# Kernel tuning notes

Measured on AMD Instinct MI355X. Metric: run time of the kernel, lower is better.

## Reference

```python
import jax, jax.numpy as jnp
import numpy as np
from jax import lax

NUM_ANCHORS = 9
NUM_CLASSES = 80
SPATIALS = [6400, 1600, 400, 100, 25]
FEATS = [80, 40, 20, 10, 5]
STRIDES = [8, 16, 32, 64, 128]
SIZES = [32, 64, 128, 256, 512]
CONF_THR = 0.6
IOU_THR = 0.5
MAX_OUT = 200
MAX_EDGE = 640.0  # max(input_size)
BATCH = 8


def _make_anchors():
    """RetinaNet-style anchors, [sum(s)*9, 4] in x1y1x2y2; anchors for one
    spatial location are contiguous, matching the reshape order in forward."""
    ratios = [0.5, 1.0, 2.0]
    scales = [1.0, 2.0 ** (1.0 / 3.0), 2.0 ** (2.0 / 3.0)]
    out = []
    for st, base, f in zip(STRIDES, SIZES, FEATS):
        wh = np.array([[base * s * np.sqrt(r), base * s / np.sqrt(r)]
                       for r in ratios for s in scales], dtype=np.float64)  # [9,2]
        c = (np.arange(f, dtype=np.float64) + 0.5) * st
        cxg, cyg = np.meshgrid(c, c)
        ctr = np.stack([cxg.ravel(), cyg.ravel()], -1)  # [f*f, 2]
        a = np.concatenate([ctr[:, None, :] - wh[None] / 2,
                            ctr[:, None, :] + wh[None] / 2], -1)  # [f*f, 9, 4]
        out.append(a.reshape(-1, 4))
    return np.concatenate(out, 0).astype(np.float32)


def setup_inputs() -> dict:
    key = jax.random.key(0)
    ks = jax.random.split(key, 10)
    inp = {}
    for i, s in enumerate(SPATIALS):
        inp[f"logits_{i}"] = jax.random.normal(ks[i], (BATCH, NUM_ANCHORS * NUM_CLASSES, s), jnp.float32)
        inp[f"regress_{i}"] = jax.random.normal(ks[5 + i], (BATCH, NUM_ANCHORS * 4, s), jnp.float32) * 0.1
    inp["anchors"] = jnp.asarray(_make_anchors())
    return inp


def _head_reshape(x, s, c):
    # [B, A*c, s] -> [B, s, A*c] -> [B, s*A, c]
    b = x.shape[0]
    return jnp.transpose(x, (0, 2, 1)).reshape(b, s * NUM_ANCHORS, c)


def _decode(anchors, deltas):
    # anchors [A,4] x1y1x2y2, deltas [B,A,4] (dx,dy,dw,dh)
    aw = anchors[:, 2] - anchors[:, 0]
    ah = anchors[:, 3] - anchors[:, 1]
    ax = anchors[:, 0] + 0.5 * aw
    ay = anchors[:, 1] + 0.5 * ah
    cx = ax + deltas[..., 0] * aw
    cy = ay + deltas[..., 1] * ah
    w = aw * jnp.exp(deltas[..., 2])
    h = ah * jnp.exp(deltas[..., 3])
    return jnp.stack([cx - 0.5 * w, cy - 0.5 * h, cx + 0.5 * w, cy + 0.5 * h], -1)


def _nms_single(scores, cats, boxes):
    # scores [A], cats [A] int, boxes [A,4]. Class-aware NMS via class offset
    # (same trick as batch_cls_nms_2d using max_edge): different classes never overlap.
    shifted = boxes + (cats.astype(boxes.dtype) * (2.0 * MAX_EDGE))[:, None]
    areas = (shifted[:, 2] - shifted[:, 0]) * (shifted[:, 3] - shifted[:, 1])
    s0 = jnp.where(scores >= CONF_THR, scores, -1.0)

    def step(s, _):
        idx = jnp.argmax(s)
        sc = s[idx]
        valid = sc > 0.0
        b = shifted[idx]
        ix1 = jnp.maximum(b[0], shifted[:, 0])
        iy1 = jnp.maximum(b[1], shifted[:, 1])
        ix2 = jnp.minimum(b[2], shifted[:, 2])
        iy2 = jnp.minimum(b[3], shifted[:, 3])
        inter = jnp.clip(ix2 - ix1, 0.0) * jnp.clip(iy2 - iy1, 0.0)
        area_b = (b[2] - b[0]) * (b[3] - b[1])
        iou = inter / (area_b + areas - inter + 1e-9)
        suppress = valid & (iou > IOU_THR)
        s = jnp.where(suppress, -1.0, s).at[idx].set(-1.0)
        return s, (idx, jnp.where(valid, sc, 0.0), valid)

    _, (idxs, scs, vs) = lax.scan(step, s0, None, length=MAX_OUT)
    vf = vs.astype(boxes.dtype)
    det_boxes = boxes[idxs] * vf[:, None]
    det_cats = jnp.where(vs, cats[idxs].astype(boxes.dtype), -1.0)
    # dets: [MAX_OUT, 6] = (x1,y1,x2,y2,score,cat); padded rows are zeros / cat=-1
    return jnp.concatenate([det_boxes, scs[:, None], det_cats[:, None]], -1)


def reference(logits_0, logits_1, logits_2, logits_3, logits_4,
              regress_0, regress_1, regress_2, regress_3, regress_4, anchors):
    logits = [logits_0, logits_1, logits_2, logits_3, logits_4]
    regress = [regress_0, regress_1, regress_2, regress_3, regress_4]
    logits = jnp.concatenate([_head_reshape(x, s, NUM_CLASSES)
                              for x, s in zip(logits, SPATIALS)], axis=1)   # [B, A, C]
    regress = jnp.concatenate([_head_reshape(x, s, 4)
                               for x, s in zip(regress, SPATIALS)], axis=1)  # [B, A, 4]
    scores = jax.nn.sigmoid(logits)                   # [B, A, C]
    sc = jnp.max(scores, axis=-1)                     # per-anchor best score
    cats = jnp.argmax(scores, axis=-1)                # per-anchor best class
    boxes = _decode(anchors, regress)                 # [B, A, 4]
    dets = jax.vmap(_nms_single)(sc, cats, boxes)     # [B, MAX_OUT, 6]
    return dets
```

## Files before the change

### kernel.cpp

```cpp
#include <hip/hip_runtime.h>
#include <cmath>

#define A_TOT 76725
#define A_PAD 76728
#define NBATCH 8
#define NCLS 80
#define NANCH 9
#define NOUT 200

#define MCAP 1024
#define NTH 1024
#define NBUCK 4096
#define CHUNK 64
#define NSLC 32
#define KBASE 0x3EC00000u
#define KSHIFT 16
#define NCHUNKS 36

__device__ __forceinline__ void decode_box(int b, int j,
                                           const float* __restrict__ rg0,
                                           const float* __restrict__ rg1,
                                           const float* __restrict__ rg2,
                                           const float* __restrict__ rg3,
                                           const float* __restrict__ rg4,
                                           const float* __restrict__ anchors,
                                           double* __restrict__ o4)
{
    int s, base;
    const float* rg;
    if (j >= 76500)      { s = 25;   base = 76500; rg = rg4; }
    else if (j >= 75600) { s = 100;  base = 75600; rg = rg3; }
    else if (j >= 72000) { s = 400;  base = 72000; rg = rg2; }
    else if (j >= 57600) { s = 1600; base = 57600; rg = rg1; }
    else                 { s = 6400; base = 0;     rg = rg0; }
    const int rem = j - base;
    const int loc = rem / 9;
    const int aa  = rem - loc * 9;
    const size_t ro = ((size_t)(b * NANCH + aa) * 4) * s + loc;
    const float f0 = rg[ro];
    const float f1 = rg[ro + (size_t)s];
    const float f2 = rg[ro + 2 * (size_t)s];
    const float f3 = rg[ro + 3 * (size_t)s];

    double d0 = (double)f0, d1 = (double)f1, d2 = (double)f2, d3 = (double)f3;
    const float4 av = *(const float4*)(anchors + (size_t)j * 4);
    double ax1 = (double)av.x, ay1 = (double)av.y;
    double ax2 = (double)av.z, ay2 = (double)av.w;
    double aw = ax2 - ax1, ah = ay2 - ay1;
    double acx = ax1 + 0.5 * aw, acy = ay1 + 0.5 * ah;
    double cx = acx + d0 * aw, cy = acy + d1 * ah;
    double w = aw * exp(d2), h = ah * exp(d3);
    o4[0] = cx - 0.5 * w;
    o4[1] = cy - 0.5 * h;
    o4[2] = cx + 0.5 * w;
    o4[3] = cy + 0.5 * h;
}

#define CMP4(vv, cc)                                            \
    do {                                                        \
        if ((vv).x > m.x) { m.x = (vv).x; mcx = (cc); }         \
        if ((vv).y > m.y) { m.y = (vv).y; mcy = (cc); }         \
        if ((vv).z > m.z) { m.z = (vv).z; mcz = (cc); }         \
        if ((vv).w > m.w) { m.w = (vv).w; mcw = (cc); }         \
    } while (0)

__global__ __launch_bounds__(512, 4)
void prep_kernel(const float* __restrict__ lg0, const float* __restrict__ lg1,
                 const float* __restrict__ lg2, const float* __restrict__ lg3,
                 const float* __restrict__ lg4,
                 unsigned* __restrict__ keys,
                 unsigned char* __restrict__ cats,
                 unsigned* __restrict__ hist)
{
    const int cx = blockIdx.x;
    const int a  = blockIdx.y;
    const int b  = blockIdx.z;
    int lvl, local;
    if (cx < 25)      { lvl = 0; local = cx; }
    else if (cx < 32) { lvl = 1; local = cx - 25; }
    else if (cx < 34) { lvl = 2; local = cx - 32; }
    else if (cx < 35) { lvl = 3; local = 0; }
    else              { lvl = 4; local = 0; }

    const int   sarr[5] = {6400, 1600, 400, 100, 25};
    const int   barr[5] = {0, 57600, 72000, 75600, 76500};
    const float* lgs[5] = {lg0, lg1, lg2, lg3, lg4};
    const int s = sarr[lvl], base = barr[lvl];
    const float* lg = lgs[lvl];

    __shared__ unsigned lh[NBUCK];
    __shared__ float4   smv[7][64];
    __shared__ int      smc[7][64][4];

    const int tid = threadIdx.x;
    for (int i = tid; i < NBUCK; i += 512) lh[i] = 0u;

    const int t2 = tid & 63;
    const int q  = tid >> 6;
    const int c0 = q * 10;
    const int locbase = local * 256 + t2 * 4;
    const bool act = locbase < s;

    float mj[4]  = {-1e30f, -1e30f, -1e30f, -1e30f};
    int   mcj[4] = {0, 0, 0, 0};

    if (act) {
        const float* lga = lg + ((size_t)(b * NANCH + a) * NCLS) * s + locbase;
        if ((s & 3) == 0) {
            const float* p  = lga + (size_t)c0 * s;
            const size_t ss = (size_t)s;
            float4 v0 = *(const float4*)(p);
            float4 v1 = *(const float4*)(p + ss);
            float4 v2 = *(const float4*)(p + 2 * ss);
            float4 v3 = *(const float4*)(p + 3 * ss);
            float4 v4 = *(const float4*)(p + 4 * ss);
            float4 v5 = *(const float4*)(p + 5 * ss);
            float4 v6 = *(const float4*)(p + 6 * ss);
            float4 v7 = *(const float4*)(p + 7 * ss);
            float4 v8 = *(const float4*)(p + 8 * ss);
            float4 v9 = *(const float4*)(p + 9 * ss);
            float4 m = v0;
            int mcx = c0, mcy = c0, mcz = c0, mcw = c0;
            CMP4(v1, c0 + 1); CMP4(v2, c0 + 2); CMP4(v3, c0 + 3);
            CMP4(v4, c0 + 4); CMP4(v5, c0 + 5); CMP4(v6, c0 + 6);
            CMP4(v7, c0 + 7); CMP4(v8, c0 + 8); CMP4(v9, c0 + 9);
            mj[0] = m.x; mj[1] = m.y; mj[2] = m.z; mj[3] = m.w;
            mcj[0] = mcx; mcj[1] = mcy; mcj[2] = mcz; mcj[3] = mcw;
        } else {
            for (int j = 0; j < 4; ++j) {
                const int loc = locbase + j;
                if (loc >= s) break;
                const float* l1 = lga + j;
                float mv = l1[(size_t)c0 * s];
                int mc = c0;
                for (int c = c0 + 1; c < c0 + 10; ++c) {
                    float v1s = l1[(size_t)c * s];
                    if (v1s > mv) { mv = v1s; mc = c; }
                }
                mj[j] = mv; mcj[j] = mc;
            }
        }
    }

    if (q > 0 && act) {
        smv[q - 1][t2] = make_float4(mj[0], mj[1], mj[2], mj[3]);
        smc[q - 1][t2][0] = mcj[0]; smc[q - 1][t2][1] = mcj[1];
        smc[q - 1][t2][2] = mcj[2]; smc[q - 1][t2][3] = mcj[3];
    }
    __syncthreads();

    if (q == 0 && act) {
        #pragma unroll
        for (int h = 0; h < 7; ++h) {
            const float4 hv4 = smv[h][t2];
            const float* hv = (const float*)&hv4;
            #pragma unroll
            for (int j = 0; j < 4; ++j) {
                if (hv[j] > mj[j]) { mj[j] = hv[j]; mcj[j] = smc[h][t2][j]; }
            }
        }
        const size_t ob = (size_t)b * A_PAD + base + (size_t)locbase * NANCH + a;
        #pragma unroll
        for (int j = 0; j < 4; ++j) {
            const int loc = locbase + j;
            if (loc >= s) continue;
            const float mv = mj[j];
            bool pass;
            if (mv >= 0.406f)      pass = true;
            else if (mv < 0.405f)  pass = false;
            else pass = (1.0 / (1.0 + exp(-(double)mv)) >= 0.6);
            unsigned kb = 0u;
            if (pass) {
                kb = __float_as_uint(mv);
                unsigned bk = (kb - KBASE) >> KSHIFT;
                if (bk > NBUCK - 1) bk = NBUCK - 1;
                atomicAdd(&lh[bk], 1u);
            }
            const size_t o = ob + (size_t)j * NANCH;
            keys[o] = kb;
            cats[o] = (unsigned char)mcj[j];
        }
    }
    __syncthreads();

    unsigned* H = hist + (size_t)b * NBUCK;
    for (int i = tid; i < NBUCK; i += 512) {
        unsigned v = lh[i];
        if (v) atomicAdd(&H[i], v);
    }
}

__global__ __launch_bounds__(256)
void compact_kernel(const unsigned* __restrict__ keys,
                    const unsigned char* __restrict__ cats,
                    const unsigned* __restrict__ hist,
                    const float* __restrict__ rg0, const float* __restrict__ rg1,
                    const float* __restrict__ rg2, const float* __restrict__ rg3,
                    const float* __restrict__ rg4,
                    const float* __restrict__ anchors,
                    unsigned long long* __restrict__ ckey,
                    double* __restrict__ cbox,
                    float* __restrict__ cscore,
                    int* __restrict__ ccount,
                    int* __restrict__ validc)
{
    const int b = blockIdx.y;
    const int tid = threadIdx.x;

    __shared__ unsigned sa[NBUCK], sb[NBUCK];
    __shared__ int bs_s;
    const unsigned* H = hist + (size_t)b * NBUCK;
    for (int i = tid; i < NBUCK; i += 256) sa[i] = H[i];
    if (tid == 0) bs_s = NBUCK;
    __syncthreads();
    unsigned* src = sa; unsigned* dst = sb;
    for (int off = 1; off < NBUCK; off <<= 1) {
        for (int i = tid; i < NBUCK; i += 256)
            dst[i] = src[i] + ((i + off < NBUCK) ? src[i + off] : 0u);
        __syncthreads();
        unsigned* t = src; src = dst; dst = t;
    }
    for (int i = tid; i < NBUCK; i += 256) {
        if (src[i] <= (unsigned)MCAP && (i == 0 || src[i - 1] > (unsigned)MCAP))
            bs_s = i;
    }
    __syncthreads();
    if (blockIdx.x == 0 && tid == 0) validc[b] = (int)src[0];
    const int bs = bs_s;

    const unsigned* K = keys + (size_t)b * A_PAD;
    const unsigned char* CT = cats + (size_t)b * A_PAD;
    const int stride = NSLC * 256;
    for (int j = blockIdx.x * 256 + tid; j < A_TOT; j += stride) {
        const unsigned k = K[j];
        if (k) {
            int bk = (int)((k - KBASE) >> KSHIFT);
            if (bk > NBUCK - 1) bk = NBUCK - 1;
            if (bk >= bs) {
                int p = atomicAdd(&ccount[b], 1);
                if (p < MCAP) {
                    unsigned pack = ((unsigned)j << 7) | (unsigned)CT[j];
                    ckey[(size_t)b * MCAP + p] =
                        ((unsigned long long)k << 24) |
                        (unsigned long long)(0xFFFFFFu - pack);
                    decode_box(b, j, rg0, rg1, rg2, rg3, rg4, anchors,
                               cbox + ((size_t)b * MCAP + p) * 4);
                    double sgd = 1.0 / (1.0 + exp(-(double)__uint_as_float(k)));
                    cscore[(size_t)b * MCAP + p] = (float)sgd;
                }
            }
        }
    }
}

__launch_bounds__(NTH, 1)
__global__ void greedy_kernel(const unsigned* __restrict__ keys,
                              const unsigned char* __restrict__ cats,
                              const float* __restrict__ rg0, const float* __restrict__ rg1,
                              const float* __restrict__ rg2, const float* __restrict__ rg3,
                              const float* __restrict__ rg4,
                              const float* __restrict__ anchors,
                              const unsigned long long* __restrict__ ckey,
                              const double* __restrict__ cbox,
                              const float* __restrict__ cscore,
                              const int* __restrict__ ccount,
                              const int* __restrict__ validc,
                              float* __restrict__ out)
{
    const int b = blockIdx.x;
    const int tid = threadIdx.x;

    __shared__ unsigned long long skey[MCAP];
    __shared__ unsigned sslot[MCAP];
    __shared__ alignas(16) char ubuf[20480];
    __shared__ int acc_s;

    const int cnt_raw = ccount[b];
    const int cnt = cnt_raw < MCAP ? cnt_raw : MCAP;
    const int valid = validc[b];

    for (int i = tid; i < MCAP; i += NTH) {
        if (i < cnt) {
            skey[i] = ckey[(size_t)b * MCAP + i];
            sslot[i] = (unsigned)i;
        } else {
            skey[i] = 0ull;
            sslot[i] = 0xFFFFFFFFu;
        }
    }
    __syncthreads();

    for (int k = 2; k <= MCAP; k <<= 1) {
        for (int j2 = k >> 1; j2 > 0; j2 >>= 1) {
            for (int i = tid; i < MCAP; i += NTH) {
                int ixj = i ^ j2;
                if (ixj > i) {
                    unsigned long long ka = skey[i], kb2 = skey[ixj];
                    unsigned pa = sslot[i], pb = sslot[ixj];
                    bool before = (ka > kb2) || (ka == kb2 && pa < pb);
                    bool dir = ((i & k) == 0);
                    if (before != dir) {
                        skey[i] = kb2; skey[ixj] = ka;
                        sslot[i] = pb; sslot[ixj] = pa;
                    }
                }
            }
            __syncthreads();
        }
    }

    double* aX1 = (double*)ubuf;
    double* aY1 = aX1 + NOUT;
    double* aX2 = aY1 + NOUT;
    double* aY2 = aX2 + NOUT;
    double* aAR = aY2 + NOUT;
    int*   aCT  = (int*)(ubuf + 8000);
    float* obuf = (float*)(ubuf + 8800);
    double* cSX1 = (double*)(ubuf + 13600);
    double* cSY1 = (double*)(ubuf + 14112);
    double* cSX2 = (double*)(ubuf + 14624);
    double* cSY2 = (double*)(ubuf + 15136);
    double* cAR2 = (double*)(ubuf + 15648);
    double (*cUB)[4] = (double(*)[4])(ubuf + 16160);
    int* cCat = (int*)(ubuf + 18208);
    unsigned long long* cMask = (unsigned long long*)(ubuf + 18464);
    int* cSup = (int*)(ubuf + 18976);
    float* cSc = (float*)(ubuf + 19232);

    for (int i = tid; i < NOUT * 6; i += NTH)
        obuf[i] = ((i % 6) == 5) ? -1.0f : 0.0f;
    __syncthreads();

    int acc = 0;
    for (int c0 = 0; c0 < cnt && acc < NOUT; c0 += CHUNK) {
        const int n = (cnt - c0) < CHUNK ? (cnt - c0) : CHUNK;

        if (tid < n) {
            unsigned long long ke = skey[c0 + tid];
            unsigned pack = 0xFFFFFFu - (unsigned)(ke & 0xFFFFFFull);
            int cat = (int)(pack & 127u);
            int sl = (int)sslot[c0 + tid];
            const double* bb = cbox + ((size_t)b * MCAP + sl) * 4;
            double b0 = bb[0], b1 = bb[1], b2 = bb[2], b3 = bb[3];
            cUB[tid][0] = b0; cUB[tid][1] = b1; cUB[tid][2] = b2; cUB[tid][3] = b3;
            double shift = (double)cat * 1280.0;
            double x1 = b0 + shift, y1 = b1 + shift;
            double x2 = b2 + shift, y2 = b3 + shift;
            cSX1[tid] = x1; cSY1[tid] = y1; cSX2[tid] = x2; cSY2[tid] = y2;
            cAR2[tid] = (x2 - x1) * (y2 - y1);
            cCat[tid] = cat;
            cSc[tid] = cscore[(size_t)b * MCAP + sl];
            cMask[tid] = 0ull;
            cSup[tid] = 0;
        }
        __syncthreads();

        {
            const int i = tid >> 4;
            if (i < n) {
                const int cat = cCat[i];
                const double x1 = cSX1[i], y1 = cSY1[i];
                const double x2 = cSX2[i], y2 = cSY2[i];
                const double areaj = cAR2[i];
                bool f = false;
                for (int r = (tid & 15); r < acc; r += 16) {
                    int cd = aCT[r] - cat; if (cd < 0) cd = -cd;
                    if (cd <= 4) {
                        double ix1 = aX1[r] > x1 ? aX1[r] : x1;
                        double iy1 = aY1[r] > y1 ? aY1[r] : y1;
                        double ix2 = aX2[r] < x2 ? aX2[r] : x2;
                        double iy2 = aY2[r] < y2 ? aY2[r] : y2;
                        double iw = ix2 - ix1; if (iw < 0.0) iw = 0.0;
                        double ih = iy2 - iy1; if (ih < 0.0) ih = 0.0;
                        double inter = iw * ih;
                        double iou = inter / (aAR[r] + areaj - inter + 1e-9);
                        if (iou > 0.5) f = true;
                    }
                }
                if (f) cSup[i] = 1;
            }
        }

        for (int p = tid; p < (n << 6); p += NTH) {
            const int i = p >> 6, j = p & 63;
            if (j < i && j < n) {
                int cd = cCat[j] - cCat[i]; if (cd < 0) cd = -cd;
                if (cd <= 4) {
                    double x1 = cSX1[i], y1 = cSY1[i];
                    double x2 = cSX2[i], y2 = cSY2[i];
                    double ix1 = cSX1[j] > x1 ? cSX1[j] : x1;
                    double iy1 = cSY1[j] > y1 ? cSY1[j] : y1;
                    double ix2 = cSX2[j] < x2 ? cSX2[j] : x2;
                    double iy2 = cSY2[j] < y2 ? cSY2[j] : y2;
                    double iw = ix2 - ix1; if (iw < 0.0) iw = 0.0;
                    double ih = iy2 - iy1; if (ih < 0.0) ih = 0.0;
                    double inter = iw * ih;
                    double iou = inter / (cAR2[j] + cAR2[i] - inter + 1e-9);
                    if (iou > 0.5)
                        atomicOr(&cMask[i], 1ull << j);
                }
            }
        }
        __syncthreads();

        if (tid < 64) {
            const int lane = tid;
            unsigned long long m = 0ull;
            int supv = 1;
            if (lane < n) { m = cMask[lane]; supv = cSup[lane]; }
            unsigned long long alive = __ballot(lane < n && !supv);
            unsigned long long am = 0ull;
            int a2 = acc;
            while (alive && a2 < NOUT) {
                int i = (int)__ffsll((unsigned long long)alive) - 1;
                am |= 1ull << i;
                ++a2;
                unsigned long long kill = __ballot((m >> i) & 1ull);
                alive &= ~(kill | (1ull << i));
            }
            if (am & (1ull << lane)) {
                int pos = acc + (int)__popcll(am & ((1ull << lane) - 1ull));
                aX1[pos] = cSX1[lane]; aY1[pos] = cSY1[lane];
                aX2[pos] = cSX2[lane]; aY2[pos] = cSY2[lane];
                aAR[pos] = cAR2[lane]; aCT[pos] = cCat[lane];
                float* o = obuf + pos * 6;
                o[0] = (float)cUB[lane][0]; o[1] = (float)cUB[lane][1];
                o[2] = (float)cUB[lane][2]; o[3] = (float)cUB[lane][3];
                o[4] = cSc[lane];
                o[5] = (float)cCat[lane];
            }
            if (lane == 0) acc_s = acc + (int)__popcll(am);
        }
        __syncthreads();
        acc = acc_s;
    }

    if (acc < NOUT && cnt < valid) {
        unsigned* rvk = (unsigned*)skey;
        int*      ri  = (int*)sslot;
        const unsigned* K = keys + (size_t)b * A_PAD;
        const unsigned char* CT = cats + (size_t)b * A_PAD;
        while (acc < NOUT) {
            unsigned best = 0u;
            int bi = 0x7fffffff;
            for (int j = tid; j < A_TOT; j += NTH) {
                const unsigned k = K[j];
                if (k) {
                    int cat = (int)CT[j];
                    double bb[4];
                    decode_box(b, j, rg0, rg1, rg2, rg3, rg4, anchors, bb);
                    double shift = (double)cat * 1280.0;
                    double x1 = bb[0] + shift, y1 = bb[1] + shift;
                    double x2 = bb[2] + shift, y2 = bb[3] + shift;
                    double areaj = (x2 - x1) * (y2 - y1);
                    bool dead = false;
                    for (int r = 0; r < acc && !dead; ++r) {
                        int cd = aCT[r] - cat; if (cd < 0) cd = -cd;
                        if (cd <= 4) {
                            double ix1 = aX1[r] > x1 ? aX1[r] : x1;
                            double iy1 = aY1[r] > y1 ? aY1[r] : y1;
                            double ix2 = aX2[r] < x2 ? aX2[r] : x2;
                            double iy2 = aY2[r] < y2 ? aY2[r] : y2;
                            double iw = ix2 - ix1; if (iw < 0.0) iw = 0.0;
                            double ih = iy2 - iy1; if (ih < 0.0) ih = 0.0;
                            double inter = iw * ih;
                            double iou = inter / (aAR[r] + areaj - inter + 1e-9);
                            if (iou > 0.5) dead = true;
                        }
                    }
                    if (!dead && k > best) { best = k; bi = j; }
                }
            }
            rvk[tid] = best; ri[tid] = bi;
            __syncthreads();
            for (int off = NTH / 2; off > 0; off >>= 1) {
                if (tid < off) {
                    if (rvk[tid + off] > rvk[tid] ||
                        (rvk[tid + off] == rvk[tid] && ri[tid + off] < ri[tid])) {
                        rvk[tid] = rvk[tid + off]; ri[tid] = ri[tid + off];
                    }
                }
                __syncthreads();
            }
            if (rvk[0] == 0u) break;
            if (tid == 0) {
                int j = ri[0];
                int cat = (int)CT[j];
                double bb[4];
                decode_box(b, j, rg0, rg1, rg2, rg3, rg4, anchors, bb);
                double shift = (double)cat * 1280.0;
                double x1 = bb[0] + shift, y1 = bb[1] + shift;
                double x2 = bb[2] + shift, y2 = bb[3] + shift;
                aX1[acc] = x1; aY1[acc] = y1; aX2[acc] = x2; aY2[acc] = y2;
                aAR[acc] = (x2 - x1) * (y2 - y1); aCT[acc] = cat;
                float* o = obuf + acc * 6;
                o[0] = (float)bb[0]; o[1] = (float)bb[1];
                o[2] = (float)bb[2]; o[3] = (float)bb[3];
                o[4] = (float)(1.0 / (1.0 + exp(-(double)__uint_as_float(rvk[0]))));
                o[5] = (float)cat;
                acc_s = acc + 1;
            }
            __syncthreads();
            acc = acc_s;
        }
    }
    __syncthreads();

    float* O = out + (size_t)b * NOUT * 6;
    for (int i = tid; i < NOUT * 6; i += NTH) O[i] = obuf[i];
}

extern "C" void kernel_launch(void* const* d_in, const int* in_sizes, int n_in,
                              void* d_out, int out_size, void* d_ws, size_t ws_size,
                              hipStream_t stream)
{
    const float* lg0 = (const float*)d_in[0];
    const float* rg0 = (const float*)d_in[1];
    const float* lg1 = (const float*)d_in[2];
    const float* rg1 = (const float*)d_in[3];
    const float* lg2 = (const float*)d_in[4];
    const float* rg2 = (const float*)d_in[5];
    const float* lg3 = (const float*)d_in[6];
    const float* rg3 = (const float*)d_in[7];
    const float* lg4 = (const float*)d_in[8];
    const float* rg4 = (const float*)d_in[9];
    const float* anchors = (const float*)d_in[10];

    char* ws = (char*)d_ws;
    unsigned*      keys   = (unsigned*)ws;
    unsigned char* cats   = (unsigned char*)(ws + 2455296);
    unsigned*      hist   = (unsigned*)(ws + 3069184);
    int*           ccount = (int*)(ws + 3200256);
    int*           validc = (int*)(ws + 3200320);
    unsigned long long* ckey = (unsigned long long*)(ws + 3200384);
    double*        cbox   = (double*)(ws + 3265920);
    float*         cscore = (float*)(ws + 3528064);

    hipMemsetAsync(hist, 0, 131072 + 32, stream);

    prep_kernel<<<dim3(NCHUNKS, NANCH, NBATCH), 512, 0, stream>>>(
        lg0, lg1, lg2, lg3, lg4, keys, cats, hist);

    compact_kernel<<<dim3(NSLC, NBATCH), 256, 0, stream>>>(
        keys, cats, hist, rg0, rg1, rg2, rg3, rg4, anchors,
        ckey, cbox, cscore, ccount, validc);

    greedy_kernel<<<NBATCH, NTH, 0, stream>>>(
        keys, cats, rg0, rg1, rg2, rg3, rg4, anchors,
        ckey, cbox, cscore, ccount, validc, (float*)d_out);
}
```

Before: 407.4 us.

## Stage high-score candidates in prep and fold compaction into greedy NMS kernel

The separate compact kernel goes away. The prep kernel now appends anchors whose max logit reaches a high fixed threshold to a small per-batch staging list, using a global atomic counter. The greedy kernel computes the histogram prefix and cutoff bucket itself, then takes candidates from the staging list when the cutoff is above the staging threshold and the list did not overflow. Otherwise it falls back to scanning all keys. This removes one launch and a full key scan, but adds global atomics in prep and serial prefix/decode work inside the 8-block greedy kernel.

```diff
diff --git a/kernel.cpp b/kernel.cpp
--- a/kernel.cpp
+++ b/kernel.cpp
@@ -12,10 +12,12 @@
 #define NTH 1024
 #define NBUCK 4096
 #define CHUNK 64
-#define NSLC 32
 #define KBASE 0x3EC00000u
 #define KSHIFT 16
 #define NCHUNKS 36
+#define SCAP 8192
+#define STAGE_THR 3.25f
+#define STAGE_BITS 0x40500000u
 
 __device__ __forceinline__ void decode_box(int b, int j,
                                            const float* __restrict__ rg0,
@@ -70,7 +72,9 @@
                  const float* __restrict__ lg4,
                  unsigned* __restrict__ keys,
                  unsigned char* __restrict__ cats,
-                 unsigned* __restrict__ hist)
+                 unsigned* __restrict__ hist,
+                 unsigned long long* __restrict__ stage,
+                 int* __restrict__ scount)
 {
     const int cx = blockIdx.x;
     const int a  = blockIdx.y;
@@ -175,6 +179,15 @@
                 unsigned bk = (kb - KBASE) >> KSHIFT;
                 if (bk > NBUCK - 1) bk = NBUCK - 1;
                 atomicAdd(&lh[bk], 1u);
+                if (mv >= STAGE_THR) {
+                    const unsigned aj = (unsigned)(base + (size_t)(locbase + j) * NANCH + a);
+                    int p = atomicAdd(&scount[b], 1);
+                    if (p < SCAP) {
+                        stage[(size_t)b * SCAP + p] =
+                            ((unsigned long long)kb << 24) |
+                            (unsigned long long)(0xFFFFFFu - ((aj << 7) | (unsigned)mcj[j]));
+                    }
+                }
             }
             const size_t o = ob + (size_t)j * NANCH;
             keys[o] = kb;
@@ -187,69 +200,6 @@
     for (int i = tid; i < NBUCK; i += 512) {
         unsigned v = lh[i];
         if (v) atomicAdd(&H[i], v);
-    }
-}
-
-__global__ __launch_bounds__(256)
-void compact_kernel(const unsigned* __restrict__ keys,
-                    const unsigned char* __restrict__ cats,
-                    const unsigned* __restrict__ hist,
-                    const float* __restrict__ rg0, const float* __restrict__ rg1,
-                    const float* __restrict__ rg2, const float* __restrict__ rg3,
-                    const float* __restrict__ rg4,
-                    const float* __restrict__ anchors,
-                    unsigned long long* __restrict__ ckey,
-                    double* __restrict__ cbox,
-                    float* __restrict__ cscore,
-                    int* __restrict__ ccount,
-                    int* __restrict__ validc)
-{
-    const int b = blockIdx.y;
-    const int tid = threadIdx.x;
-
-    __shared__ unsigned sa[NBUCK], sb[NBUCK];
-    __shared__ int bs_s;
-    const unsigned* H = hist + (size_t)b * NBUCK;
-    for (int i = tid; i < NBUCK; i += 256) sa[i] = H[i];
-    if (tid == 0) bs_s = NBUCK;
-    __syncthreads();
-    unsigned* src = sa; unsigned* dst = sb;
-    for (int off = 1; off < NBUCK; off <<= 1) {
-        for (int i = tid; i < NBUCK; i += 256)
-            dst[i] = src[i] + ((i + off < NBUCK) ? src[i + off] : 0u);
-        __syncthreads();
-        unsigned* t = src; src = dst; dst = t;
-    }
-    for (int i = tid; i < NBUCK; i += 256) {
-        if (src[i] <= (unsigned)MCAP && (i == 0 || src[i - 1] > (unsigned)MCAP))
-            bs_s = i;
-    }
-    __syncthreads();
-    if (blockIdx.x == 0 && tid == 0) validc[b] = (int)src[0];
-    const int bs = bs_s;
-
-    const unsigned* K = keys + (size_t)b * A_PAD;
-    const unsigned char* CT = cats + (size_t)b * A_PAD;
-    const int stride = NSLC * 256;
-    for (int j = blockIdx.x * 256 + tid; j < A_TOT; j += stride) {
-        const unsigned k = K[j];
-        if (k) {
-            int bk = (int)((k - KBASE) >> KSHIFT);
-            if (bk > NBUCK - 1) bk = NBUCK - 1;
-            if (bk >= bs) {
-                int p = atomicAdd(&ccount[b], 1);
-                if (p < MCAP) {
-                    unsigned pack = ((unsigned)j << 7) | (unsigned)CT[j];
-                    ckey[(size_t)b * MCAP + p] =
-                        ((unsigned long long)k << 24) |
-                        (unsigned long long)(0xFFFFFFu - pack);
-                    decode_box(b, j, rg0, rg1, rg2, rg3, rg4, anchors,
-                               cbox + ((size_t)b * MCAP + p) * 4);
-                    double sgd = 1.0 / (1.0 + exp(-(double)__uint_as_float(k)));
-                    cscore[(size_t)b * MCAP + p] = (float)sgd;
-                }
-            }
-        }
     }
 }
 
@@ -260,29 +210,96 @@
                               const float* __restrict__ rg2, const float* __restrict__ rg3,
                               const float* __restrict__ rg4,
                               const float* __restrict__ anchors,
-                              const unsigned long long* __restrict__ ckey,
-                              const double* __restrict__ cbox,
-                              const float* __restrict__ cscore,
-                              const int* __restrict__ ccount,
-                              const int* __restrict__ validc,
+                              const unsigned* __restrict__ hist,
+                              const unsigned long long* __restrict__ stage,
+                              const int* __restrict__ scount,
+                              double* __restrict__ cbox,
+                              float* __restrict__ cscore,
                               float* __restrict__ out)
 {
     const int b = blockIdx.x;
     const int tid = threadIdx.x;
 
-    __shared__ unsigned long long skey[MCAP];
-    __shared__ unsigned sslot[MCAP];
-    __shared__ alignas(16) char ubuf[20480];
-    __shared__ int acc_s;
-
-    const int cnt_raw = ccount[b];
+    __shared__ alignas(16) char pool[33280];
+    __shared__ int bs_sh, valid_sh, cnt_sh, acc_s;
+
+    const unsigned* K = keys + (size_t)b * A_PAD;
+    const unsigned char* CT = cats + (size_t)b * A_PAD;
+
+    {
+        unsigned* sa = (unsigned*)pool;
+        unsigned* sb = (unsigned*)(pool + 16384);
+        const unsigned* H = hist + (size_t)b * NBUCK;
+        for (int i = tid; i < NBUCK; i += NTH) sa[i] = H[i];
+        if (tid == 0) bs_sh = NBUCK;
+        __syncthreads();
+        unsigned* src = sa; unsigned* dst = sb;
+        for (int off = 1; off < NBUCK; off <<= 1) {
+            for (int i = tid; i < NBUCK; i += NTH)
+                dst[i] = src[i] + ((i + off < NBUCK) ? src[i + off] : 0u);
+            __syncthreads();
+            unsigned* t = src; src = dst; dst = t;
+        }
+        for (int i = tid; i < NBUCK; i += NTH) {
+            if (src[i] <= (unsigned)MCAP && (i == 0 || src[i - 1] > (unsigned)MCAP))
+                bs_sh = i;
+        }
+        __syncthreads();
+        if (tid == 0) { valid_sh = (int)src[0]; cnt_sh = 0; }
+        __syncthreads();
+    }
+    const int bs = bs_sh;
+    const int valid = valid_sh;
+
+    unsigned long long* skey = (unsigned long long*)pool;
+    unsigned* sslot = (unsigned*)(pool + 8192);
+    char* ubuf = pool + 12288;
+
+    {
+        const unsigned Lb = KBASE + ((unsigned)bs << KSHIFT);
+        const int S = scount[b];
+        const bool trust = (S <= SCAP) && (Lb >= STAGE_BITS);
+        if (trust) {
+            for (int i = tid; i < S; i += NTH) {
+                unsigned long long e = stage[(size_t)b * SCAP + i];
+                if ((unsigned)(e >> 24) >= Lb) {
+                    int p = atomicAdd(&cnt_sh, 1);
+                    if (p < MCAP) skey[p] = e;
+                }
+            }
+        } else {
+            for (int j = tid; j < A_TOT; j += NTH) {
+                const unsigned k = K[j];
+                if (k) {
+                    int bk = (int)((k - KBASE) >> KSHIFT);
+                    if (bk > NBUCK - 1) bk = NBUCK - 1;
+                    if (bk >= bs) {
+                        int p = atomicAdd(&cnt_sh, 1);
+                        if (p < MCAP) {
+                            unsigned pack = ((unsigned)j << 7) | (unsigned)CT[j];
+                            skey[p] = ((unsigned long long)k << 24) |
+                                      (unsigned long long)(0xFFFFFFu - pack);
+                        }
+                    }
+                }
+            }
+        }
+        __syncthreads();
+    }
+    const int cnt_raw = cnt_sh;
     const int cnt = cnt_raw < MCAP ? cnt_raw : MCAP;
-    const int valid = validc[b];
 
     for (int i = tid; i < MCAP; i += NTH) {
         if (i < cnt) {
-            skey[i] = ckey[(size_t)b * MCAP + i];
             sslot[i] = (unsigned)i;
+            unsigned long long e = skey[i];
+            unsigned kb = (unsigned)(e >> 24);
+            unsigned pack = 0xFFFFFFu - (unsigned)(e & 0xFFFFFFull);
+            int j = (int)(pack >> 7);
+            decode_box(b, j, rg0, rg1, rg2, rg3, rg4, anchors,
+                       cbox + ((size_t)b * MCAP + i) * 4);
+            double sgd = 1.0 / (1.0 + exp(-(double)__uint_as_float(kb)));
+            cscore[(size_t)b * MCAP + i] = (float)sgd;
         } else {
             skey[i] = 0ull;
             sslot[i] = 0xFFFFFFFFu;
@@ -438,8 +455,6 @@
     if (acc < NOUT && cnt < valid) {
         unsigned* rvk = (unsigned*)skey;
         int*      ri  = (int*)sslot;
-        const unsigned* K = keys + (size_t)b * A_PAD;
-        const unsigned char* CT = cats + (size_t)b * A_PAD;
         while (acc < NOUT) {
             unsigned best = 0u;
             int bi = 0x7fffffff;
@@ -530,22 +545,17 @@
     unsigned*      keys   = (unsigned*)ws;
     unsigned char* cats   = (unsigned char*)(ws + 2455296);
     unsigned*      hist   = (unsigned*)(ws + 3069184);
-    int*           ccount = (int*)(ws + 3200256);
-    int*           validc = (int*)(ws + 3200320);
-    unsigned long long* ckey = (unsigned long long*)(ws + 3200384);
-    double*        cbox   = (double*)(ws + 3265920);
-    float*         cscore = (float*)(ws + 3528064);
+    int*           scount = (int*)(ws + 3200256);
+    unsigned long long* stage = (unsigned long long*)(ws + 3200512);
+    double*        cbox   = (double*)(ws + 3724800);
+    float*         cscore = (float*)(ws + 3986944);
 
     hipMemsetAsync(hist, 0, 131072 + 32, stream);
 
     prep_kernel<<<dim3(NCHUNKS, NANCH, NBATCH), 512, 0, stream>>>(
-        lg0, lg1, lg2, lg3, lg4, keys, cats, hist);
-
-    compact_kernel<<<dim3(NSLC, NBATCH), 256, 0, stream>>>(
-        keys, cats, hist, rg0, rg1, rg2, rg3, rg4, anchors,
-        ckey, cbox, cscore, ccount, validc);
+        lg0, lg1, lg2, lg3, lg4, keys, cats, hist, stage, scount);
 
     greedy_kernel<<<NBATCH, NTH, 0, stream>>>(
         keys, cats, rg0, rg1, rg2, rg3, rg4, anchors,
-        ckey, cbox, cscore, ccount, validc, (float*)d_out);
+        hist, stage, scount, cbox, cscore, (float*)d_out);
 }
```

New measurement: 387.3 us. 4.9% less time.
